# Kernel tuning notes

Measured on AMD Instinct MI355X. Metric: run time of the kernel, lower is better.

## Reference

```python
import jax, jax.numpy as jnp
import numpy as np

B, N, D = 4, 1024, 1024      # batch, seq_len, d_model
H, DK, DV = 16, 64, 64       # n_head, d_k, d_v


def setup_inputs() -> dict:
    key = jax.random.key(0)
    ks = jax.random.split(key, 6)
    xavier = (2.0 / (D + DK)) ** 0.5  # xavier_normal_ std for (d_model, d_k) fan
    return {
        "q": jax.random.normal(ks[0], (B, N, D), jnp.float32),
        "k": jax.random.normal(ks[1], (B, N, D), jnp.float32),
        "v": jax.random.normal(ks[2], (B, N, D), jnp.float32),
        "weight_qs": xavier * jax.random.normal(ks[3], (H, D, DK), jnp.float32),
        "weight_ks": xavier * jax.random.normal(ks[4], (H, D, DK), jnp.float32),
        "weight_vs": xavier * jax.random.normal(ks[5], (H, D, DV), jnp.float32),
    }


def reference(q, k, v, weight_qs, weight_ks, weight_vs):
    # Per-head projections (torch: repeat batch over heads + bmm with (H,D,DK) weights)
    h, d_model, d_k = weight_qs.shape
    scale = 1.0 / (d_k ** 0.5)
    qh = jnp.einsum('bnd,hdk->hbnk', q, weight_qs)   # (H,B,N,DK)
    kh = jnp.einsum('bmd,hdk->hbmk', k, weight_ks)   # (H,B,M,DK)
    vh = jnp.einsum('bmd,hdv->hbmv', v, weight_vs)   # (H,B,M,DV)
    scores = jnp.einsum('hbnk,hbmk->hbnm', qh, kh) * scale  # (H,B,N,M)
    attn = jax.nn.softmax(scores, axis=-1)
    # dropout is identity in eval/deterministic mode
    out = jnp.einsum('hbnm,hbmv->hbnv', attn, vh)    # (H,B,N,DV)
    # torch: split head-stacked batch dim and cat along feature dim -> (B,N,H*DV)
    out = jnp.transpose(out, (1, 2, 0, 3)).reshape(out.shape[1], out.shape[2], -1)
    attn = attn.reshape(h * attn.shape[1], attn.shape[2], attn.shape[3])  # (H*B,N,M)
    return out, attn
```

## Files before the change

kernel.cpp:

```cpp
#include <hip/hip_runtime.h>

typedef short short8 __attribute__((ext_vector_type(8)));
typedef short short4_ __attribute__((ext_vector_type(4)));
typedef float f32x4 __attribute__((ext_vector_type(4)));

#define GLD16(gsrc, ldst) \
  __builtin_amdgcn_global_load_lds((__attribute__((address_space(1))) const void*)(gsrc), \
                                   (__attribute__((address_space(3))) void*)(ldst), 16, 0, 0)

#define BAR() do { asm volatile("s_waitcnt lgkmcnt(0)" ::: "memory"); \
  __builtin_amdgcn_sched_barrier(0); __builtin_amdgcn_s_barrier(); } while (0)

static __device__ __forceinline__ short f2bf(float f) {
  union { float f; unsigned u; } x; x.f = f;
  unsigned r = x.u + 0x7fffu + ((x.u >> 16) & 1u);
  return (short)(r >> 16);
}
static __device__ __forceinline__ float bf2f(unsigned short h) {
  union { unsigned u; float f; } x; x.u = ((unsigned)h) << 16;
  return x.f;
}

__global__ __launch_bounds__(256) void cast_pack(
    const float* __restrict__ q, const float* __restrict__ k, const float* __restrict__ v,
    const float* __restrict__ wq, const float* __restrict__ wk, const float* __restrict__ wv,
    short* __restrict__ xq, short* __restrict__ xk, short* __restrict__ xv,
    short* __restrict__ oq, short* __restrict__ ok, short* __restrict__ ov) {
  int z = blockIdx.z;
  if (blockIdx.x < 4096) {
    const float* s = (z == 0) ? q : (z == 1) ? k : v;
    short* d = (z == 0) ? xq : (z == 1) ? xk : xv;
    int i = (blockIdx.x * 256 + threadIdx.x) * 4;
    float4 f = *(const float4*)(s + i);
    short4_ o;
    o[0] = f2bf(f.x); o[1] = f2bf(f.y); o[2] = f2bf(f.z); o[3] = f2bf(f.w);
    *(short4_*)(d + i) = o;
  } else {
    const float* W = (z == 0) ? wq : (z == 1) ? wk : wv;
    int c = blockIdx.x - 4096;
    short* o = ((z == 0) ? oq : (z == 1) ? ok : ov) + (size_t)c * 1024;
    int h = c >> 6, kk = c & 63;
    const float* src = W + (size_t)h * 65536 + kk;
    #pragma unroll
    for (int it = 0; it < 4; ++it) {
      int d = it * 256 + threadIdx.x;
      o[d] = f2bf(src[(size_t)d * 64]);
    }
  }
}

__global__ __launch_bounds__(256) void proj_gemm(
    const short* __restrict__ xq, const short* __restrict__ xk, const short* __restrict__ xv,
    const short* __restrict__ wq, const short* __restrict__ wk, const short* __restrict__ wv,
    short* __restrict__ pq, short* __restrict__ pk, short* __restrict__ pv) {
  int z = blockIdx.z;
  const short* A  = (z == 0) ? xq : (z == 1) ? xk : xv;
  const short* Bt = (z == 0) ? wq : (z == 1) ? wk : wv;
  short* C        = (z == 0) ? pq : (z == 1) ? pk : pv;
  __shared__ __attribute__((aligned(16))) short As[2][128 * 32];
  __shared__ __attribute__((aligned(16))) short Bs[2][128 * 32];
  int t = threadIdx.x, l = t & 63, w = t >> 6;
  int wr = w >> 1, wc = w & 1;
  int lr = l & 15, lk = l >> 4;
  int bm0 = blockIdx.y * 128, bn0 = blockIdx.x * 128;
  const f32x4 Z = {0.f, 0.f, 0.f, 0.f};
  f32x4 acc[4][4];
  #pragma unroll
  for (int m = 0; m < 4; ++m)
    #pragma unroll
    for (int n = 0; n < 4; ++n) acc[m][n] = Z;

  int boff0 = w * 2 * 1024 + l * 16;
  int row0 = boff0 >> 6, ke0 = (boff0 & 63) >> 1;
  int boff1 = boff0 + 1024;
  int row1 = boff1 >> 6, ke1 = (boff1 & 63) >> 1;
  const short* ga0 = A + (size_t)(bm0 + row0) * 1024 + ke0;
  const short* ga1 = A + (size_t)(bm0 + row1) * 1024 + ke1;
  const short* gb0 = Bt + (size_t)(bn0 + row0) * 1024 + ke0;
  const short* gb1 = Bt + (size_t)(bn0 + row1) * 1024 + ke1;
  int lo = (w * 2) * 512, lo1 = (w * 2 + 1) * 512;

  for (int kb = 0; kb < 1024; kb += 64) {
    #pragma unroll
    for (int hh = 0; hh < 2; ++hh) {
      int kc = kb + hh * 32;
      GLD16(ga0 + kc, As[hh] + lo);
      GLD16(ga1 + kc, As[hh] + lo1);
      GLD16(gb0 + kc, Bs[hh] + lo);
      GLD16(gb1 + kc, Bs[hh] + lo1);
    }
    __syncthreads();
    #pragma unroll
    for (int hh = 0; hh < 2; ++hh) {
      short8 a[4], bfr[4];
      #pragma unroll
      for (int m = 0; m < 4; ++m)
        a[m] = *(const short8*)(As[hh] + (wr * 64 + m * 16 + lr) * 32 + lk * 8);
      #pragma unroll
      for (int n = 0; n < 4; ++n)
        bfr[n] = *(const short8*)(Bs[hh] + (wc * 64 + n * 16 + lr) * 32 + lk * 8);
      __builtin_amdgcn_s_setprio(1);
      #pragma unroll
      for (int m = 0; m < 4; ++m)
        #pragma unroll
        for (int n = 0; n < 4; ++n)
          acc[m][n] = __builtin_amdgcn_mfma_f32_16x16x32_bf16(a[m], bfr[n], acc[m][n], 0, 0, 0);
      __builtin_amdgcn_s_setprio(0);
    }
    __syncthreads();
  }
  #pragma unroll
  for (int m = 0; m < 4; ++m)
    #pragma unroll
    for (int n = 0; n < 4; ++n)
      #pragma unroll
      for (int i = 0; i < 4; ++i) {
        int r = bm0 + wr * 64 + m * 16 + lk * 4 + i;
        int cc = bn0 + wc * 64 + n * 16 + lr;
        C[(size_t)r * 1024 + cc] = f2bf(acc[m][n][i]);
      }
}

__global__ __launch_bounds__(256) void vtrans(
    const short* __restrict__ pv, short* __restrict__ vt) {
  __shared__ short T[64 * 72];
  int t = threadIdx.x;
  int hb = blockIdx.y, h = hb >> 2, b = hb & 3;
  int n0 = blockIdx.x * 64;
  const short* src = pv + (size_t)b * 1048576 + (size_t)n0 * 1024 + h * 64;
  #pragma unroll
  for (int it = 0; it < 2; ++it) {
    int id = it * 256 + t;
    int row = id >> 3, seg = id & 7;
    *(short8*)(T + row * 72 + seg * 8) = *(const short8*)(src + (size_t)row * 1024 + seg * 8);
  }
  __syncthreads();
  short* dst = vt + (size_t)hb * 65536 + n0;
  #pragma unroll
  for (int it = 0; it < 2; ++it) {
    int id = it * 256 + t;
    int dv = id >> 3, seg = id & 7;
    short8 vv;
    #pragma unroll
    for (int jj = 0; jj < 8; ++jj) vv[jj] = T[(seg * 8 + jj) * 72 + dv];
    *(short8*)(dst + (size_t)dv * 1024 + seg * 8) = vv;
  }
}

__global__ __launch_bounds__(512) void attn_fused(
    const short* __restrict__ pq, const short* __restrict__ pk, const short* __restrict__ vt,
    float* __restrict__ dout) {
  __shared__ __attribute__((aligned(16))) short Ks[2][64 * 64];
  __shared__ __attribute__((aligned(16))) short Vs[2][64 * 64];
  __shared__ __attribute__((aligned(16))) short Ps[128 * 64];
  int t = threadIdx.x, l = t & 63, w = t >> 6;
  int lr = l & 15, lk = l >> 4;
  int r7 = lr & 7;
  int bid = blockIdx.x;
  int swz = (bid & 7) * 64 + (bid >> 3);
  int hb = swz >> 3, qt = swz & 7;
  int h = hb >> 2, b = hb & 3;
  int q0 = qt * 128;
  const short* Qg = pq + (size_t)b * 1048576 + h * 64;
  const short* Kg = pk + (size_t)b * 1048576 + h * 64;
  const short* Vt = vt + (size_t)hb * 65536;
  float* attnp = dout + 4194304 + (size_t)hb * 1048576;
  const f32x4 Z = {0.f, 0.f, 0.f, 0.f};
  const float scale = 0.125f;
  int r0 = w * 16;
  int sj = t >> 3, slt = t & 7;
  int stoff = sj * 64 + ((slt ^ (sj & 7)) << 3);

  const short* qrow = Qg + (size_t)(q0 + r0 + lr) * 1024;
  short8 aq[2];
  aq[0] = *(const short8*)(qrow + lk * 8);
  aq[1] = *(const short8*)(qrow + 32 + lk * 8);

  short8 ka, va;
  ka = *(const short8*)(Kg + (size_t)sj * 1024 + slt * 8);
  *(short8*)(Ks[0] + stoff) = ka;
  BAR();

  float s = 0.0f;

  for (int nc = 0; nc < 16; ++nc) {
    int cur = nc & 1;
    if (nc < 15)
      ka = *(const short8*)(Kg + (size_t)((nc + 1) * 64 + sj) * 1024 + slt * 8);
    f32x4 acc[4] = {Z, Z, Z, Z};
    __builtin_amdgcn_s_setprio(1);
    #pragma unroll
    for (int kk = 0; kk < 2; ++kk)
      #pragma unroll
      for (int n = 0; n < 4; ++n) {
        short8 bk = *(const short8*)(Ks[cur] + (n * 16 + lr) * 64 + (((kk * 4 + lk) ^ r7) << 3));
        acc[n] = __builtin_amdgcn_mfma_f32_16x16x32_bf16(bk, aq[kk], acc[n], 0, 0, 0);
      }
    __builtin_amdgcn_s_setprio(0);
    #pragma unroll
    for (int n = 0; n < 4; ++n)
      s += __expf(acc[n][0] * scale) + __expf(acc[n][1] * scale) +
           __expf(acc[n][2] * scale) + __expf(acc[n][3] * scale);
    if (nc < 15)
      *(short8*)(Ks[cur ^ 1] + stoff) = ka;
    BAR();
  }
  s += __shfl_xor(s, 16, 64);
  s += __shfl_xor(s, 32, 64);
  float inv = 1.0f / s;

  ka = *(const short8*)(Kg + (size_t)sj * 1024 + slt * 8);
  va = *(const short8*)(Vt + (size_t)sj * 1024 + slt * 8);
  *(short8*)(Ks[0] + stoff) = ka;
  *(short8*)(Vs[0] + stoff) = va;
  BAR();

  f32x4 acco[4] = {Z, Z, Z, Z};
  float* arow = attnp + (size_t)(q0 + r0 + lr) * 1024 + lk * 4;
  short* psrow = Ps + (r0 + lr) * 64;
  int wsw = (lr & 7) << 1;
  for (int nc = 0; nc < 16; ++nc) {
    int cur = nc & 1;
    if (nc < 15) {
      ka = *(const short8*)(Kg + (size_t)((nc + 1) * 64 + sj) * 1024 + slt * 8);
      va = *(const short8*)(Vt + (size_t)sj * 1024 + (nc + 1) * 64 + slt * 8);
    }
    f32x4 acc[4] = {Z, Z, Z, Z};
    __builtin_amdgcn_s_setprio(1);
    #pragma unroll
    for (int kk = 0; kk < 2; ++kk)
      #pragma unroll
      for (int n = 0; n < 4; ++n) {
        short8 bk = *(const short8*)(Ks[cur] + (n * 16 + lr) * 64 + (((kk * 4 + lk) ^ r7) << 3));
        acc[n] = __builtin_amdgcn_mfma_f32_16x16x32_bf16(bk, aq[kk], acc[n], 0, 0, 0);
      }
    __builtin_amdgcn_s_setprio(0);
    #pragma unroll
    for (int n = 0; n < 4; ++n) {
      float e0 = __expf(acc[n][0] * scale) * inv;
      float e1 = __expf(acc[n][1] * scale) * inv;
      float e2 = __expf(acc[n][2] * scale) * inv;
      float e3 = __expf(acc[n][3] * scale) * inv;
      float4 fo = {e0, e1, e2, e3};
      *(float4*)(arow + nc * 64 + n * 16) = fo;
      short4_ p4;
      p4[0] = f2bf(e0); p4[1] = f2bf(e1); p4[2] = f2bf(e2); p4[3] = f2bf(e3);
      *(short4_*)(psrow + (((n * 4 + lk) ^ wsw) << 2)) = p4;
    }
    #pragma unroll
    for (int kk = 0; kk < 2; ++kk) {
      short8 ap = *(const short8*)(psrow + (((kk * 4 + lk) ^ r7) << 3));
      __builtin_amdgcn_s_setprio(1);
      #pragma unroll
      for (int f = 0; f < 4; ++f) {
        short8 bv = *(const short8*)(Vs[cur] + (f * 16 + lr) * 64 + (((kk * 4 + lk) ^ r7) << 3));
        acco[f] = __builtin_amdgcn_mfma_f32_16x16x32_bf16(ap, bv, acco[f], 0, 0, 0);
      }
      __builtin_amdgcn_s_setprio(0);
    }
    if (nc < 15) {
      *(short8*)(Ks[cur ^ 1] + stoff) = ka;
      *(short8*)(Vs[cur ^ 1] + stoff) = va;
    }
    BAR();
  }
  #pragma unroll
  for (int f = 0; f < 4; ++f)
    #pragma unroll
    for (int i = 0; i < 4; ++i) {
      int row = q0 + r0 + lk * 4 + i;
      int dv = f * 16 + lr;
      dout[(size_t)b * 1048576 + (size_t)row * 1024 + h * 64 + dv] = acco[f][i];
    }
}

extern "C" void kernel_launch(void* const* d_in, const int* in_sizes, int n_in,
                              void* d_out, int out_size, void* d_ws, size_t ws_size,
                              hipStream_t stream) {
  const void* big[3] = {0, 0, 0};
  const void* small[3] = {0, 0, 0};
  int nb = 0, ns = 0;
  for (int i = 0; i < n_in && i < 6; ++i) {
    if (in_sizes[i] == 4194304) { if (nb < 3) big[nb++] = d_in[i]; }
    else                        { if (ns < 3) small[ns++] = d_in[i]; }
  }
  const float *q, *k, *v, *wq, *wk, *wv;
  if (nb == 3 && ns == 3) {
    q = (const float*)big[0]; k = (const float*)big[1]; v = (const float*)big[2];
    wq = (const float*)small[0]; wk = (const float*)small[1]; wv = (const float*)small[2];
  } else {
    q = (const float*)d_in[0]; k = (const float*)d_in[1]; v = (const float*)d_in[2];
    wq = (const float*)d_in[3]; wk = (const float*)d_in[4]; wv = (const float*)d_in[5];
  }
  short* W   = (short*)d_ws;
  short* xq  = W;
  short* xk  = W + 4194304;
  short* xv  = W + 8388608;
  short* wtq = W + 12582912;
  short* wtk = W + 13631488;
  short* wtv = W + 14680064;
  short* pq  = W + 15728640;
  short* pk  = W + 19922944;
  short* pv  = W + 24117248;
  short* vt  = W + 28311552;
  float* out = (float*)d_out;

  cast_pack<<<dim3(5120, 1, 3), 256, 0, stream>>>(q, k, v, wq, wk, wv,
                                                  xq, xk, xv, wtq, wtk, wtv);
  proj_gemm<<<dim3(8, 32, 3), 256, 0, stream>>>(xq, xk, xv, wtq, wtk, wtv, pq, pk, pv);
  vtrans<<<dim3(16, 64), 256, 0, stream>>>(pv, vt);
  attn_fused<<<dim3(512), 512, 0, stream>>>(pq, pk, vt, out);
}
```

Baseline: 156.9 us.

## Halve attention block threads, give each wave two 16-row query tiles

The fused attention kernel now launches 256 threads (4 waves) per block instead of 512, and each wave computes two 16-row query tiles that share every K and V fragment read from LDS. Each thread stages two 16-byte chunks of the K/V tiles per iteration instead of one. This halves LDS fragment reads per MFMA and cuts the number of waves waiting at each barrier. In exchange it doubles accumulator registers per thread and lowers the wave count per block, which may reduce latency hiding for the heavy fp32 attention-matrix stores.

```diff
diff --git a/kernel.cpp b/kernel.cpp
--- a/kernel.cpp
+++ b/kernel.cpp
@@ -147,7 +147,7 @@
   }
 }
 
-__global__ __launch_bounds__(512) void attn_fused(
+__global__ __launch_bounds__(256) void attn_fused(
     const short* __restrict__ pq, const short* __restrict__ pk, const short* __restrict__ vt,
     float* __restrict__ dout) {
   __shared__ __attribute__((aligned(16))) short Ks[2][64 * 64];
@@ -167,100 +167,138 @@
   float* attnp = dout + 4194304 + (size_t)hb * 1048576;
   const f32x4 Z = {0.f, 0.f, 0.f, 0.f};
   const float scale = 0.125f;
-  int r0 = w * 16;
-  int sj = t >> 3, slt = t & 7;
-  int stoff = sj * 64 + ((slt ^ (sj & 7)) << 3);
-
-  const short* qrow = Qg + (size_t)(q0 + r0 + lr) * 1024;
-  short8 aq[2];
-  aq[0] = *(const short8*)(qrow + lk * 8);
-  aq[1] = *(const short8*)(qrow + 32 + lk * 8);
-
-  short8 ka, va;
-  ka = *(const short8*)(Kg + (size_t)sj * 1024 + slt * 8);
-  *(short8*)(Ks[0] + stoff) = ka;
+  int r0 = w * 32;
+  int sj = t >> 2, s0 = (t & 3) * 2, s1 = s0 + 1;
+  int stoff0 = sj * 64 + ((s0 ^ (sj & 7)) << 3);
+  int stoff1 = sj * 64 + ((s1 ^ (sj & 7)) << 3);
+
+  const short* qrowA = Qg + (size_t)(q0 + r0 + lr) * 1024;
+  const short* qrowB = Qg + (size_t)(q0 + r0 + 16 + lr) * 1024;
+  short8 aqA[2], aqB[2];
+  aqA[0] = *(const short8*)(qrowA + lk * 8);
+  aqA[1] = *(const short8*)(qrowA + 32 + lk * 8);
+  aqB[0] = *(const short8*)(qrowB + lk * 8);
+  aqB[1] = *(const short8*)(qrowB + 32 + lk * 8);
+
+  short8 ka0, ka1, va0, va1;
+  ka0 = *(const short8*)(Kg + (size_t)sj * 1024 + s0 * 8);
+  ka1 = *(const short8*)(Kg + (size_t)sj * 1024 + s1 * 8);
+  *(short8*)(Ks[0] + stoff0) = ka0;
+  *(short8*)(Ks[0] + stoff1) = ka1;
   BAR();
 
-  float s = 0.0f;
+  float sA = 0.0f, sB = 0.0f;
 
   for (int nc = 0; nc < 16; ++nc) {
     int cur = nc & 1;
-    if (nc < 15)
-      ka = *(const short8*)(Kg + (size_t)((nc + 1) * 64 + sj) * 1024 + slt * 8);
-    f32x4 acc[4] = {Z, Z, Z, Z};
+    if (nc < 15) {
+      ka0 = *(const short8*)(Kg + (size_t)((nc + 1) * 64 + sj) * 1024 + s0 * 8);
+      ka1 = *(const short8*)(Kg + (size_t)((nc + 1) * 64 + sj) * 1024 + s1 * 8);
+    }
+    f32x4 accA[4] = {Z, Z, Z, Z}, accB[4] = {Z, Z, Z, Z};
     __builtin_amdgcn_s_setprio(1);
     #pragma unroll
     for (int kk = 0; kk < 2; ++kk)
       #pragma unroll
       for (int n = 0; n < 4; ++n) {
         short8 bk = *(const short8*)(Ks[cur] + (n * 16 + lr) * 64 + (((kk * 4 + lk) ^ r7) << 3));
-        acc[n] = __builtin_amdgcn_mfma_f32_16x16x32_bf16(bk, aq[kk], acc[n], 0, 0, 0);
+        accA[n] = __builtin_amdgcn_mfma_f32_16x16x32_bf16(bk, aqA[kk], accA[n], 0, 0, 0);
+        accB[n] = __builtin_amdgcn_mfma_f32_16x16x32_bf16(bk, aqB[kk], accB[n], 0, 0, 0);
       }
     __builtin_amdgcn_s_setprio(0);
     #pragma unroll
-    for (int n = 0; n < 4; ++n)
-      s += __expf(acc[n][0] * scale) + __expf(acc[n][1] * scale) +
-           __expf(acc[n][2] * scale) + __expf(acc[n][3] * scale);
-    if (nc < 15)
-      *(short8*)(Ks[cur ^ 1] + stoff) = ka;
+    for (int n = 0; n < 4; ++n) {
+      sA += __expf(accA[n][0] * scale) + __expf(accA[n][1] * scale) +
+            __expf(accA[n][2] * scale) + __expf(accA[n][3] * scale);
+      sB += __expf(accB[n][0] * scale) + __expf(accB[n][1] * scale) +
+            __expf(accB[n][2] * scale) + __expf(accB[n][3] * scale);
+    }
+    if (nc < 15) {
+      *(short8*)(Ks[cur ^ 1] + stoff0) = ka0;
+      *(short8*)(Ks[cur ^ 1] + stoff1) = ka1;
+    }
     BAR();
   }
-  s += __shfl_xor(s, 16, 64);
-  s += __shfl_xor(s, 32, 64);
-  float inv = 1.0f / s;
-
-  ka = *(const short8*)(Kg + (size_t)sj * 1024 + slt * 8);
-  va = *(const short8*)(Vt + (size_t)sj * 1024 + slt * 8);
-  *(short8*)(Ks[0] + stoff) = ka;
-  *(short8*)(Vs[0] + stoff) = va;
+  sA += __shfl_xor(sA, 16, 64);
+  sA += __shfl_xor(sA, 32, 64);
+  sB += __shfl_xor(sB, 16, 64);
+  sB += __shfl_xor(sB, 32, 64);
+  float invA = 1.0f / sA, invB = 1.0f / sB;
+
+  ka0 = *(const short8*)(Kg + (size_t)sj * 1024 + s0 * 8);
+  ka1 = *(const short8*)(Kg + (size_t)sj * 1024 + s1 * 8);
+  va0 = *(const short8*)(Vt + (size_t)sj * 1024 + s0 * 8);
+  va1 = *(const short8*)(Vt + (size_t)sj * 1024 + s1 * 8);
+  *(short8*)(Ks[0] + stoff0) = ka0;
+  *(short8*)(Ks[0] + stoff1) = ka1;
+  *(short8*)(Vs[0] + stoff0) = va0;
+  *(short8*)(Vs[0] + stoff1) = va1;
   BAR();
 
-  f32x4 acco[4] = {Z, Z, Z, Z};
-  float* arow = attnp + (size_t)(q0 + r0 + lr) * 1024 + lk * 4;
-  short* psrow = Ps + (r0 + lr) * 64;
+  f32x4 accoA[4] = {Z, Z, Z, Z}, accoB[4] = {Z, Z, Z, Z};
+  float* arowA = attnp + (size_t)(q0 + r0 + lr) * 1024 + lk * 4;
+  float* arowB = attnp + (size_t)(q0 + r0 + 16 + lr) * 1024 + lk * 4;
+  short* psrowA = Ps + (r0 + lr) * 64;
+  short* psrowB = Ps + (r0 + 16 + lr) * 64;
   int wsw = (lr & 7) << 1;
   for (int nc = 0; nc < 16; ++nc) {
     int cur = nc & 1;
     if (nc < 15) {
-      ka = *(const short8*)(Kg + (size_t)((nc + 1) * 64 + sj) * 1024 + slt * 8);
-      va = *(const short8*)(Vt + (size_t)sj * 1024 + (nc + 1) * 64 + slt * 8);
-    }
-    f32x4 acc[4] = {Z, Z, Z, Z};
+      ka0 = *(const short8*)(Kg + (size_t)((nc + 1) * 64 + sj) * 1024 + s0 * 8);
+      ka1 = *(const short8*)(Kg + (size_t)((nc + 1) * 64 + sj) * 1024 + s1 * 8);
+      va0 = *(const short8*)(Vt + (size_t)sj * 1024 + (nc + 1) * 64 + s0 * 8);
+      va1 = *(const short8*)(Vt + (size_t)sj * 1024 + (nc + 1) * 64 + s1 * 8);
+    }
+    f32x4 accA[4] = {Z, Z, Z, Z}, accB[4] = {Z, Z, Z, Z};
     __builtin_amdgcn_s_setprio(1);
     #pragma unroll
     for (int kk = 0; kk < 2; ++kk)
       #pragma unroll
       for (int n = 0; n < 4; ++n) {
         short8 bk = *(const short8*)(Ks[cur] + (n * 16 + lr) * 64 + (((kk * 4 + lk) ^ r7) << 3));
-        acc[n] = __builtin_amdgcn_mfma_f32_16x16x32_bf16(bk, aq[kk], acc[n], 0, 0, 0);
+        accA[n] = __builtin_amdgcn_mfma_f32_16x16x32_bf16(bk, aqA[kk], accA[n], 0, 0, 0);
+        accB[n] = __builtin_amdgcn_mfma_f32_16x16x32_bf16(bk, aqB[kk], accB[n], 0, 0, 0);
       }
     __builtin_amdgcn_s_setprio(0);
     #pragma unroll
     for (int n = 0; n < 4; ++n) {
-      float e0 = __expf(acc[n][0] * scale) * inv;
-      float e1 = __expf(acc[n][1] * scale) * inv;
-      float e2 = __expf(acc[n][2] * scale) * inv;
-      float e3 = __expf(acc[n][3] * scale) * inv;
-      float4 fo = {e0, e1, e2, e3};
-      *(float4*)(arow + nc * 64 + n * 16) = fo;
-      short4_ p4;
-      p4[0] = f2bf(e0); p4[1] = f2bf(e1); p4[2] = f2bf(e2); p4[3] = f2bf(e3);
-      *(short4_*)(psrow + (((n * 4 + lk) ^ wsw) << 2)) = p4;
+      float a0 = __expf(accA[n][0] * scale) * invA;
+      float a1 = __expf(accA[n][1] * scale) * invA;
+      float a2 = __expf(accA[n][2] * scale) * invA;
+      float a3 = __expf(accA[n][3] * scale) * invA;
+      float4 foA = {a0, a1, a2, a3};
+      *(float4*)(arowA + nc * 64 + n * 16) = foA;
+      short4_ pA;
+      pA[0] = f2bf(a0); pA[1] = f2bf(a1); pA[2] = f2bf(a2); pA[3] = f2bf(a3);
+      *(short4_*)(psrowA + (((n * 4 + lk) ^ wsw) << 2)) = pA;
+      float b0 = __expf(accB[n][0] * scale) * invB;
+      float b1 = __expf(accB[n][1] * scale) * invB;
+      float b2 = __expf(accB[n][2] * scale) * invB;
+      float b3 = __expf(accB[n][3] * scale) * invB;
+      float4 foB = {b0, b1, b2, b3};
+      *(float4*)(arowB + nc * 64 + n * 16) = foB;
+      short4_ pB;
+      pB[0] = f2bf(b0); pB[1] = f2bf(b1); pB[2] = f2bf(b2); pB[3] = f2bf(b3);
+      *(short4_*)(psrowB + (((n * 4 + lk) ^ wsw) << 2)) = pB;
     }
     #pragma unroll
     for (int kk = 0; kk < 2; ++kk) {
-      short8 ap = *(const short8*)(psrow + (((kk * 4 + lk) ^ r7) << 3));
+      short8 apA = *(const short8*)(psrowA + (((kk * 4 + lk) ^ r7) << 3));
+      short8 apB = *(const short8*)(psrowB + (((kk * 4 + lk) ^ r7) << 3));
       __builtin_amdgcn_s_setprio(1);
       #pragma unroll
       for (int f = 0; f < 4; ++f) {
         short8 bv = *(const short8*)(Vs[cur] + (f * 16 + lr) * 64 + (((kk * 4 + lk) ^ r7) << 3));
-        acco[f] = __builtin_amdgcn_mfma_f32_16x16x32_bf16(ap, bv, acco[f], 0, 0, 0);
+        accoA[f] = __builtin_amdgcn_mfma_f32_16x16x32_bf16(apA, bv, accoA[f], 0, 0, 0);
+        accoB[f] = __builtin_amdgcn_mfma_f32_16x16x32_bf16(apB, bv, accoB[f], 0, 0, 0);
       }
       __builtin_amdgcn_s_setprio(0);
     }
     if (nc < 15) {
-      *(short8*)(Ks[cur ^ 1] + stoff) = ka;
-      *(short8*)(Vs[cur ^ 1] + stoff) = va;
+      *(short8*)(Ks[cur ^ 1] + stoff0) = ka0;
+      *(short8*)(Ks[cur ^ 1] + stoff1) = ka1;
+      *(short8*)(Vs[cur ^ 1] + stoff0) = va0;
+      *(short8*)(Vs[cur ^ 1] + stoff1) = va1;
     }
     BAR();
   }
@@ -268,9 +306,10 @@
   for (int f = 0; f < 4; ++f)
     #pragma unroll
     for (int i = 0; i < 4; ++i) {
-      int row = q0 + r0 + lk * 4 + i;
+      int rowA = q0 + r0 + lk * 4 + i;
       int dv = f * 16 + lr;
-      dout[(size_t)b * 1048576 + (size_t)row * 1024 + h * 64 + dv] = acco[f][i];
+      dout[(size_t)b * 1048576 + (size_t)rowA * 1024 + h * 64 + dv] = accoA[f][i];
+      dout[(size_t)b * 1048576 + (size_t)(rowA + 16) * 1024 + h * 64 + dv] = accoB[f][i];
     }
 }
 
@@ -309,5 +348,5 @@
                                                   xq, xk, xv, wtq, wtk, wtv);
   proj_gemm<<<dim3(8, 32, 3), 256, 0, stream>>>(xq, xk, xv, wtq, wtk, wtv, pq, pk, pv);
   vtrans<<<dim3(16, 64), 256, 0, stream>>>(pv, vt);
-  attn_fused<<<dim3(512), 512, 0, stream>>>(pq, pk, vt, out);
-}
+  attn_fused<<<dim3(512), 256, 0, stream>>>(pq, pk, vt, out);
+}
```

Measured after the change: 159.9 us. Within noise of the previous version (+1.9%).
